# Kernel tuning notes

Hardware: AMD Instinct MI355X
Metric: run time of the kernel (lower is better)

Reference implementation:

```python
import jax, jax.numpy as jnp
import numpy as np

DIM = 768; HEADS = 12; HD = DIM // HEADS; W0 = 14; W1 = 14
NT = W0 * W1; N = NT + 1; HID = 4 * DIM; B = 64
SCALE = HD ** -0.5; EPS = 1e-6


def _rel_indices():
    # replicates DecoupledRelativePositionBias index buffers
    def rel1d(s):
        i = np.arange(s)
        return i[None, :] - i[:, None] + s - 1  # [s, s]
    h = rel1d(W0).reshape(W0, 1, W0, 1) * np.ones((1, W1, 1, W1), np.int64)
    h = (rel1d(W0).reshape(W0, 1, W0, 1) + np.zeros((1, W1, 1, W1), np.int64)).reshape(NT, NT)
    w = (rel1d(W1).reshape(1, W1, 1, W1) + np.zeros((W0, 1, W0, 1), np.int64)).reshape(NT, NT)
    def add_cls(idx, off):
        new = np.zeros((N, N), np.int64)
        new[1:, 1:] = idx
        new[0, :] = off
        new[:, 0] = off + 1
        new[0, 0] = off + 2
        return new
    return add_cls(h, 2 * W0 - 1), add_cls(w, 2 * W1 - 1)


def setup_inputs() -> dict:
    key = jax.random.key(0)
    ks = jax.random.split(key, 10)
    hi, wi = _rel_indices()
    s = 0.02
    return {
        "x": jax.random.normal(ks[0], (B, N, DIM), jnp.float32),
        "norm1_w": jnp.ones((DIM,), jnp.float32),
        "norm1_b": jnp.zeros((DIM,), jnp.float32),
        "qkv_w": jax.random.normal(ks[1], (3 * DIM, DIM), jnp.float32) * s,
        "q_bias": jax.random.normal(ks[2], (DIM,), jnp.float32) * s,
        "v_bias": jax.random.normal(ks[3], (DIM,), jnp.float32) * s,
        "proj_w": jax.random.normal(ks[4], (DIM, DIM), jnp.float32) * s,
        "proj_b": jnp.zeros((DIM,), jnp.float32),
        "rpb_high": jax.random.normal(ks[5], (2 * W0 + 2, HEADS), jnp.float32) * s,
        "rpb_width": jax.random.normal(ks[6], (2 * W1 + 2, HEADS), jnp.float32) * s,
        "norm2_w": jnp.ones((DIM,), jnp.float32),
        "norm2_b": jnp.zeros((DIM,), jnp.float32),
        "fc1_w": jax.random.normal(ks[7], (HID, DIM), jnp.float32) * s,
        "fc1_b": jnp.zeros((HID,), jnp.float32),
        "fc2_w": jax.random.normal(ks[8], (DIM, HID), jnp.float32) * s,
        "fc2_b": jnp.zeros((DIM,), jnp.float32),
        "high_idx": jnp.asarray(hi, jnp.int32),
        "width_idx": jnp.asarray(wi, jnp.int32),
    }


def _ln(x, w, b):
    mu = x.mean(-1, keepdims=True)
    var = x.var(-1, keepdims=True)  # population variance, matching unbiased=False
    return (x - mu) * jax.lax.rsqrt(var + EPS) * w + b


def reference(x, norm1_w, norm1_b, qkv_w, q_bias, v_bias, proj_w, proj_b,
              rpb_high, rpb_width, norm2_w, norm2_b, fc1_w, fc1_b, fc2_w, fc2_b,
              high_idx, width_idx):
    b, n, c = x.shape
    # --- attention branch ---
    h = _ln(x, norm1_w, norm1_b)
    qkv_bias = jnp.concatenate([q_bias, jnp.zeros_like(q_bias), v_bias])
    qkv = h @ qkv_w.T + qkv_bias                      # [B, N, 3C]
    qkv = qkv.reshape(b, n, 3, HEADS, HD).transpose(2, 0, 3, 1, 4)
    q, k, v = qkv[0] * SCALE, qkv[1], qkv[2]          # [B, H, N, hd]
    attn = jnp.einsum('bhqd,bhkd->bhqk', q.astype(jnp.float32), k.astype(jnp.float32))
    # decoupled relative position bias: two embedding gathers + add
    bias = (rpb_high[high_idx] + rpb_width[width_idx]).transpose(2, 0, 1)  # [H, N, N]
    attn = attn + bias[None].astype(attn.dtype)
    attn = jax.nn.softmax(attn, axis=-1).astype(x.dtype)
    out = jnp.einsum('bhqk,bhkd->bhqd', attn, v)
    out = out.transpose(0, 2, 1, 3).reshape(b, n, c)
    x = x + (out @ proj_w.T + proj_b)
    # --- MLP branch ---
    h2 = _ln(x, norm2_w, norm2_b)
    m = jax.nn.gelu(h2 @ fc1_w.T + fc1_b, approximate=False)
    x = x + (m @ fc2_w.T + fc2_b)
    return x
```

## Files before the change

kernel.cpp:

```cpp
#include <hip/hip_runtime.h>
#include <hip/hip_bf16.h>
#include <cstdint>

#define DIM   768
#define HEADS 12
#define HD    64
#define NTOK  197
#define BATCH 64
#define MROWS (BATCH*NTOK)
#define MPAD  12672
#define HIDN  3072
#define QSCALE 0.125f
#define LNEPS 1e-6f

typedef __bf16 bf16;
typedef __bf16 bf16x8 __attribute__((ext_vector_type(8)));
typedef __bf16 bf16x4 __attribute__((ext_vector_type(4)));
typedef float  f32x4  __attribute__((ext_vector_type(4)));

__device__ inline void gload_lds16(const void* src, void* dst) {
  __builtin_amdgcn_global_load_lds(
      (__attribute__((address_space(1))) void*)(src),
      (__attribute__((address_space(3))) void*)(dst), 16, 0, 0);
}

__global__ __launch_bounds__(256) void conv_kernel(const float* __restrict__ in,
                                                   bf16* __restrict__ out, int n4) {
  int i = blockIdx.x * 256 + threadIdx.x;
  if (i < n4) {
    float4 f = ((const float4*)in)[i];
    bf16x4 o; o.x = (bf16)f.x; o.y = (bf16)f.y; o.z = (bf16)f.z; o.w = (bf16)f.w;
    ((bf16x4*)out)[i] = o;
  }
}

__global__ __launch_bounds__(256) void bias_kernel(const float* __restrict__ rh,
                                                   const float* __restrict__ rw,
                                                   const int* __restrict__ hidx,
                                                   const int* __restrict__ widx,
                                                   float* __restrict__ bias) {
  int idx = blockIdx.x * 256 + threadIdx.x;
  const int NN = NTOK * NTOK;
  if (idx >= HEADS * NN) return;
  int h  = idx / NN;
  int ij = idx - h * NN;
  bias[idx] = rh[hidx[ij] * HEADS + h] + rw[widx[ij] * HEADS + h];
}

__global__ __launch_bounds__(256) void ln_kernel(const float* __restrict__ x,
                                                 const float* __restrict__ w,
                                                 const float* __restrict__ b,
                                                 bf16* __restrict__ out) {
  int row = blockIdx.x;
  int tid = threadIdx.x;
  const float* xr = x + (size_t)row * DIM;
  float v0 = xr[tid], v1 = xr[tid + 256], v2 = xr[tid + 512];
  float s  = v0 + v1 + v2;
  float s2 = v0 * v0 + v1 * v1 + v2 * v2;
#pragma unroll
  for (int d = 1; d < 64; d <<= 1) { s += __shfl_xor(s, d); s2 += __shfl_xor(s2, d); }
  __shared__ float red[8];
  int wv = tid >> 6, ln = tid & 63;
  if (ln == 0) { red[wv] = s; red[wv + 4] = s2; }
  __syncthreads();
  s  = red[0] + red[1] + red[2] + red[3];
  s2 = red[4] + red[5] + red[6] + red[7];
  float mean = s * (1.0f / DIM);
  float var  = s2 * (1.0f / DIM) - mean * mean;
  float rs   = rsqrtf(var + LNEPS);
  bf16* outr = out + (size_t)row * DIM;
  outr[tid]       = (bf16)((v0 - mean) * rs * w[tid]       + b[tid]);
  outr[tid + 256] = (bf16)((v1 - mean) * rs * w[tid + 256] + b[tid + 256]);
  outr[tid + 512] = (bf16)((v2 - mean) * rs * w[tid + 512] + b[tid + 512]);
}

template <int EPI>
__global__ __launch_bounds__(256, 3)
void gemm128(const bf16* __restrict__ A, const bf16* __restrict__ Bw,
             int K, int Ncols, int Ntiles,
             const float* __restrict__ p0, const float* __restrict__ p1,
             void* __restrict__ outp) {
  __shared__ __align__(16) bf16 As[128 * 64];
  __shared__ __align__(16) bf16 Bs[128 * 64];
  const int tid  = threadIdx.x;
  const int wave = tid >> 6, lane = tid & 63;
  const int wm = wave >> 1, wn = wave & 1;
  const int lr16 = lane & 15, hi16 = lane >> 4;

  const int nwg = gridDim.x;
  const int q8 = nwg >> 3, r8 = nwg & 7;
  const int xcd = blockIdx.x & 7, jj8 = blockIdx.x >> 3;
  const int chunk = (xcd < r8 ? xcd * (q8 + 1) : r8 * (q8 + 1) + (xcd - r8) * q8) + jj8;
  const int mt = chunk / Ntiles, nt = chunk - mt * Ntiles;
  const int rowBase = mt * 128;
  const int colBase = nt * 128;
  const size_t Kb = (size_t)K * 2;
  const int KT = K >> 6;

  const int s7 = lr16 & 7;
  const int colk0 = (hi16 ^ s7) * 16;
  const int colk1 = ((4 + hi16) ^ s7) * 16;
  const int rowb_a = (wm * 64 + lr16) * 128;
  const int rowb_b = (wn * 64 + lr16) * 128;

  const int srow = wave * 8 + (lane >> 3);
  const int scb  = (((lane & 7) ^ ((lane >> 3) & 7)) * 16);
  const char* aSrcP[4];
  const char* bSrcP[4];
#pragma unroll
  for (int r = 0; r < 4; ++r) {
    int ra = rowBase + r * 32 + srow;
    if (ra > MROWS - 1) ra = MROWS - 1;
    aSrcP[r] = (const char*)A + (size_t)ra * Kb + scb;
    bSrcP[r] = (const char*)Bw + (size_t)(colBase + r * 32 + srow) * Kb + scb;
  }

  f32x4 acc[4][4] = {};

  for (int t = 0; t < KT; ++t) {
    const size_t koff = (size_t)t * 128;
#pragma unroll
    for (int r = 0; r < 4; ++r)
      gload_lds16(aSrcP[r] + koff, (char*)As + (r * 32 + wave * 8) * 128);
#pragma unroll
    for (int r = 0; r < 4; ++r)
      gload_lds16(bSrcP[r] + koff, (char*)Bs + (r * 32 + wave * 8) * 128);
    __syncthreads();

    bf16x8 bfr[4][2];
#pragma unroll
    for (int n = 0; n < 4; ++n) {
      bfr[n][0] = *(const bf16x8*)((const char*)Bs + rowb_b + n * 2048 + colk0);
      bfr[n][1] = *(const bf16x8*)((const char*)Bs + rowb_b + n * 2048 + colk1);
    }
#pragma unroll
    for (int m = 0; m < 4; ++m) {
      bf16x8 a0 = *(const bf16x8*)((const char*)As + rowb_a + m * 2048 + colk0);
      bf16x8 a1 = *(const bf16x8*)((const char*)As + rowb_a + m * 2048 + colk1);
#pragma unroll
      for (int n = 0; n < 4; ++n) {
        acc[m][n] = __builtin_amdgcn_mfma_f32_16x16x32_bf16(a0, bfr[n][0], acc[m][n], 0, 0, 0);
        acc[m][n] = __builtin_amdgcn_mfma_f32_16x16x32_bf16(a1, bfr[n][1], acc[m][n], 0, 0, 0);
      }
    }
    __syncthreads();
  }

  const int rl = hi16 * 4;
  const int cl = lr16;
#pragma unroll
  for (int m = 0; m < 4; ++m) {
#pragma unroll
    for (int n = 0; n < 4; ++n) {
#pragma unroll
      for (int r = 0; r < 4; ++r) {
        int row = rowBase + wm * 64 + m * 16 + rl + r;
        int col = colBase + wn * 64 + n * 16 + cl;
        if (row >= MROWS) continue;
        float v = acc[m][n][r];
        if constexpr (EPI == 0) {
          int which = col / DIM;
          int jj = col - which * DIM;
          if (which == 0) v = (v + p0[jj]) * QSCALE;
          else if (which == 2) v = v + p1[jj];
          int bb = row / NTOK, nt2 = row - bb * NTOK;
          int h = jj >> 6, hd = jj & 63;
          ((bf16*)outp)[((size_t)(which * 768 + bb * HEADS + h) * NTOK + nt2) * 64 + hd] = (bf16)v;
        } else if constexpr (EPI == 1) {
          ((float*)outp)[(size_t)row * Ncols + col] =
              p1[(size_t)row * Ncols + col] + v + p0[col];
        } else {
          float t2 = v + p0[col];
          float g = 0.5f * t2 * (1.0f + erff(t2 * 0.70710678118654752f));
          ((bf16*)outp)[(size_t)row * Ncols + col] = (bf16)g;
        }
      }
    }
  }
}

#define VTS 232
__global__ __launch_bounds__(256, 4)
void attn_kernel(const bf16* __restrict__ qkv, const float* __restrict__ bias,
                 bf16* __restrict__ out) {
  const int bh = blockIdx.x;
  const int b = bh / HEADS, h = bh - b * HEADS;
  const bf16* qg = qkv + (size_t)bh * NTOK * HD;
  const bf16* kg = qg + (size_t)768 * NTOK * HD;
  const bf16* vg = qg + (size_t)1536 * NTOK * HD;

  __shared__ __align__(16) bf16 Vt[64 * VTS];
  __shared__ __align__(16) bf16 Ps[4][2][16 * 40];

  const int tid = threadIdx.x;
  for (int i = tid; i < NTOK * HD; i += 256) {
    int j = i >> 6, d = i & 63;
    Vt[d * VTS + j] = vg[i];
  }
  for (int i = tid; i < 64 * (VTS - NTOK); i += 256) {
    int d = i / (VTS - NTOK), j = NTOK + (i - d * (VTS - NTOK));
    Vt[d * VTS + j] = (bf16)0.0f;
  }
  __syncthreads();

  const int wave = tid >> 6, lane = tid & 63;
  const int lr = lane & 15, lg = lane >> 4;
  const int tstart = (wave == 0) ? 0 : 1 + wave * 3;
  const int tcount = (wave == 0) ? 4 : 3;
  const float* bh_bias = bias + (size_t)h * NTOK * NTOK;

  for (int ti = 0; ti < tcount; ++ti) {
    const int mi = tstart + ti;
    int qrow = mi * 16 + lr; if (qrow > NTOK - 1) qrow = NTOK - 1;
    bf16x8 aq0 = *(const bf16x8*)(qg + (size_t)qrow * 64 + lg * 8);
    bf16x8 aq1 = *(const bf16x8*)(qg + (size_t)qrow * 64 + 32 + lg * 8);

    f32x4 oacc[4] = {};
    float m[4] = {-1e30f, -1e30f, -1e30f, -1e30f};
    float l[4] = {0.f, 0.f, 0.f, 0.f};
    const int ivb = (mi * 16 + lg * 4 < NTOK) ? mi * 16 + lg * 4 : NTOK - 1;

#pragma unroll 1
    for (int kt = 0; kt < 7; ++kt) {
      const int j0 = kt * 32 + lr;
      const bf16* kp0 = kg + (size_t)(kt * 32 + lr) * 64 + lg * 8;
      const bf16* kp1 = kp0 + (size_t)16 * 64;
      f32x4 s0 = {}, s1 = {};
      s0 = __builtin_amdgcn_mfma_f32_16x16x32_bf16(aq0, *(const bf16x8*)kp0, s0, 0, 0, 0);
      s0 = __builtin_amdgcn_mfma_f32_16x16x32_bf16(aq1, *(const bf16x8*)(kp0 + 32), s0, 0, 0, 0);
      s1 = __builtin_amdgcn_mfma_f32_16x16x32_bf16(aq0, *(const bf16x8*)kp1, s1, 0, 0, 0);
      s1 = __builtin_amdgcn_mfma_f32_16x16x32_bf16(aq1, *(const bf16x8*)(kp1 + 32), s1, 0, 0, 0);

      bf16* buf = &Ps[wave][kt & 1][0];
#pragma unroll
      for (int r = 0; r < 4; ++r) {
        int iv = ivb + r; if (iv > NTOK - 1) iv = NTOK - 1;
        float sv0 = (j0 < NTOK)      ? s0[r] + bh_bias[(size_t)iv * NTOK + j0]      : -1e30f;
        float sv1 = (j0 + 16 < NTOK) ? s1[r] + bh_bias[(size_t)iv * NTOK + j0 + 16] : -1e30f;
        float cmax = fmaxf(sv0, sv1);
#pragma unroll
        for (int d = 1; d < 16; d <<= 1) cmax = fmaxf(cmax, __shfl_xor(cmax, d));
        float mnew = fmaxf(m[r], cmax);
        float scale = __expf(m[r] - mnew);
        m[r] = mnew;
        float e0 = __expf(sv0 - mnew);
        float e1 = __expf(sv1 - mnew);
        l[r] = l[r] * scale + e0 + e1;
#pragma unroll
        for (int nd = 0; nd < 4; ++nd) oacc[nd][r] *= scale;
        buf[(lg * 4 + r) * 40 + lr]      = (bf16)e0;
        buf[(lg * 4 + r) * 40 + 16 + lr] = (bf16)e1;
      }
      asm volatile("s_waitcnt lgkmcnt(0)" ::: "memory");
      __builtin_amdgcn_sched_barrier(0);
      bf16x8 pa = *(const bf16x8*)&buf[lr * 40 + lg * 8];
#pragma unroll
      for (int nd = 0; nd < 4; ++nd) {
        bf16x8 bv = *(const bf16x8*)&Vt[(nd * 16 + lr) * VTS + kt * 32 + lg * 8];
        oacc[nd] = __builtin_amdgcn_mfma_f32_16x16x32_bf16(pa, bv, oacc[nd], 0, 0, 0);
      }
    }

    float rowinv[4];
#pragma unroll
    for (int r = 0; r < 4; ++r) {
      float ls = l[r];
#pragma unroll
      for (int d = 1; d < 16; d <<= 1) ls += __shfl_xor(ls, d);
      rowinv[r] = 1.0f / ls;
    }

    bf16* Ob = &Ps[wave][0][0];
#pragma unroll
    for (int nd = 0; nd < 4; ++nd)
#pragma unroll
      for (int r = 0; r < 4; ++r)
        Ob[(lg * 4 + r) * 72 + nd * 16 + lr] = (bf16)(oacc[nd][r] * rowinv[r]);
    asm volatile("s_waitcnt lgkmcnt(0)" ::: "memory");
    __builtin_amdgcn_sched_barrier(0);
    const int rows = NTOK - mi * 16;
#pragma unroll
    for (int pass = 0; pass < 2; ++pass) {
      int orow = pass * 8 + (lane >> 3);
      if (orow < rows) {
        bf16x8 v = *(const bf16x8*)&Ob[orow * 72 + (lane & 7) * 8];
        *(bf16x8*)(out + (size_t)(b * NTOK + mi * 16 + orow) * DIM + h * 64 + (lane & 7) * 8) = v;
      }
    }
  }
}

extern "C" void kernel_launch(void* const* d_in, const int* in_sizes, int n_in,
                              void* d_out, int out_size, void* d_ws, size_t ws_size,
                              hipStream_t stream) {
  const float* x    = (const float*)d_in[0];
  const float* n1w  = (const float*)d_in[1];
  const float* n1b  = (const float*)d_in[2];
  const float* qkvw = (const float*)d_in[3];
  const float* qb   = (const float*)d_in[4];
  const float* vb   = (const float*)d_in[5];
  const float* pw   = (const float*)d_in[6];
  const float* pb   = (const float*)d_in[7];
  const float* rh   = (const float*)d_in[8];
  const float* rw   = (const float*)d_in[9];
  const float* n2w  = (const float*)d_in[10];
  const float* n2b  = (const float*)d_in[11];
  const float* f1w  = (const float*)d_in[12];
  const float* f1b  = (const float*)d_in[13];
  const float* f2w  = (const float*)d_in[14];
  const float* f2b  = (const float*)d_in[15];
  const int* hidx   = (const int*)d_in[16];
  const int* widx   = (const int*)d_in[17];

  char* ws = (char*)d_ws;
  size_t off = 0;
  auto alloc = [&](size_t bytes) {
    void* p = ws + off;
    off += (bytes + 255) & ~(size_t)255;
    return p;
  };
  bf16* wqkv  = (bf16*)alloc((size_t)2304 * 768 * 2);
  bf16* wproj = (bf16*)alloc((size_t)768 * 768 * 2);
  bf16* wfc1  = (bf16*)alloc((size_t)3072 * 768 * 2);
  bf16* wfc2  = (bf16*)alloc((size_t)768 * 3072 * 2);
  float* biasT = (float*)alloc((size_t)HEADS * NTOK * NTOK * 4);
  bf16* hbf = (bf16*)alloc((size_t)MROWS * 768 * 2);
  float* x1 = (float*)alloc((size_t)MROWS * 768 * 4);
  char* region = (char*)alloc((size_t)MPAD * HIDN * 2);
  bf16* qkv   = (bf16*)region;
  bf16* attno = (bf16*)(region + (size_t)2304 * NTOK * 64 * 2);
  bf16* mbuf  = (bf16*)region;

  conv_kernel<<<(2304 * 768 / 4 + 255) / 256, 256, 0, stream>>>(qkvw, wqkv, 2304 * 768 / 4);
  conv_kernel<<<(768 * 768 / 4 + 255) / 256, 256, 0, stream>>>(pw, wproj, 768 * 768 / 4);
  conv_kernel<<<(3072 * 768 / 4 + 255) / 256, 256, 0, stream>>>(f1w, wfc1, 3072 * 768 / 4);
  conv_kernel<<<(768 * 3072 / 4 + 255) / 256, 256, 0, stream>>>(f2w, wfc2, 768 * 3072 / 4);
  bias_kernel<<<(HEADS * NTOK * NTOK + 255) / 256, 256, 0, stream>>>(rh, rw, hidx, widx, biasT);

  const int MT = MPAD / 128;
  ln_kernel<<<MROWS, 256, 0, stream>>>(x, n1w, n1b, hbf);
  gemm128<0><<<MT * 18, 256, 0, stream>>>(hbf, wqkv, 768, 2304, 18, qb, vb, qkv);
  attn_kernel<<<768, 256, 0, stream>>>(qkv, biasT, attno);
  gemm128<1><<<MT * 6, 256, 0, stream>>>(attno, wproj, 768, 768, 6, pb, x, x1);
  ln_kernel<<<MROWS, 256, 0, stream>>>(x1, n2w, n2b, hbf);
  gemm128<2><<<MT * 24, 256, 0, stream>>>(hbf, wfc1, 768, HIDN, 24, f1b, nullptr, mbuf);
  gemm128<1><<<MT * 6, 256, 0, stream>>>(mbuf, wfc2, HIDN, 768, 6, f2b, x1, d_out);
}
```

Baseline: 433.8 us.

## Double-buffer GEMM A tiles and widen attention to eight waves with bias prefetch

The GEMM now double-buffers the A tile in LDS, issuing the next A load before computing the current tile. It uses explicit vmcnt waits and raw barriers, and raises wave priority around the MFMA block. The attention kernel moves to 512 threads (8 waves) with interleaved query-tile assignment, prefetches the next key tile's bias values into registers, and skips the online-softmax rescale when the max does not grow. These changes aim to hide global-load latency and balance work across waves, at the cost of more LDS and register pressure.

```diff
diff --git a/kernel.cpp b/kernel.cpp
--- a/kernel.cpp
+++ b/kernel.cpp
@@ -23,6 +23,12 @@
       (__attribute__((address_space(1))) void*)(src),
       (__attribute__((address_space(3))) void*)(dst), 16, 0, 0);
 }
+
+#define BAR()      asm volatile("s_barrier" ::: "memory")
+#define WAIT_LGKM0() do { asm volatile("s_waitcnt lgkmcnt(0)" ::: "memory"); \
+                          __builtin_amdgcn_sched_barrier(0); } while (0)
+#define WAIT_VM(n) do { asm volatile("s_waitcnt vmcnt(" #n ")" ::: "memory"); \
+                        __builtin_amdgcn_sched_barrier(0); } while (0)
 
 __global__ __launch_bounds__(256) void conv_kernel(const float* __restrict__ in,
                                                    bf16* __restrict__ out, int n4) {
@@ -80,7 +86,7 @@
              int K, int Ncols, int Ntiles,
              const float* __restrict__ p0, const float* __restrict__ p1,
              void* __restrict__ outp) {
-  __shared__ __align__(16) bf16 As[128 * 64];
+  __shared__ __align__(16) bf16 As[2][128 * 64];
   __shared__ __align__(16) bf16 Bs[128 * 64];
   const int tid  = threadIdx.x;
   const int wave = tid >> 6, lane = tid & 63;
@@ -115,35 +121,58 @@
     bSrcP[r] = (const char*)Bw + (size_t)(colBase + r * 32 + srow) * Kb + scb;
   }
 
-  f32x4 acc[4][4] = {};
-
-  for (int t = 0; t < KT; ++t) {
+  auto stageA = [&](int t, int buf) {
     const size_t koff = (size_t)t * 128;
 #pragma unroll
     for (int r = 0; r < 4; ++r)
-      gload_lds16(aSrcP[r] + koff, (char*)As + (r * 32 + wave * 8) * 128);
+      gload_lds16(aSrcP[r] + koff, (char*)&As[buf][0] + (r * 32 + wave * 8) * 128);
+  };
+  auto stageB = [&](int t) {
+    const size_t koff = (size_t)t * 128;
 #pragma unroll
     for (int r = 0; r < 4; ++r)
       gload_lds16(bSrcP[r] + koff, (char*)Bs + (r * 32 + wave * 8) * 128);
-    __syncthreads();
-
+  };
+
+  f32x4 acc[4][4] = {};
+
+  stageA(0, 0);
+  int cur = 0;
+  for (int t = 0; t < KT; ++t) {
+    stageB(t);
+    if (t + 1 < KT) {
+      stageA(t + 1, cur ^ 1);
+      WAIT_VM(4);
+    } else {
+      WAIT_VM(0);
+    }
+    BAR();
+
+    const char* Ab = (const char*)&As[cur][0];
     bf16x8 bfr[4][2];
 #pragma unroll
     for (int n = 0; n < 4; ++n) {
       bfr[n][0] = *(const bf16x8*)((const char*)Bs + rowb_b + n * 2048 + colk0);
       bfr[n][1] = *(const bf16x8*)((const char*)Bs + rowb_b + n * 2048 + colk1);
     }
+    bf16x8 afr[4][2];
 #pragma unroll
     for (int m = 0; m < 4; ++m) {
-      bf16x8 a0 = *(const bf16x8*)((const char*)As + rowb_a + m * 2048 + colk0);
-      bf16x8 a1 = *(const bf16x8*)((const char*)As + rowb_a + m * 2048 + colk1);
+      afr[m][0] = *(const bf16x8*)(Ab + rowb_a + m * 2048 + colk0);
+      afr[m][1] = *(const bf16x8*)(Ab + rowb_a + m * 2048 + colk1);
+    }
+    WAIT_LGKM0();
+    __builtin_amdgcn_s_setprio(1);
+#pragma unroll
+    for (int m = 0; m < 4; ++m)
 #pragma unroll
       for (int n = 0; n < 4; ++n) {
-        acc[m][n] = __builtin_amdgcn_mfma_f32_16x16x32_bf16(a0, bfr[n][0], acc[m][n], 0, 0, 0);
-        acc[m][n] = __builtin_amdgcn_mfma_f32_16x16x32_bf16(a1, bfr[n][1], acc[m][n], 0, 0, 0);
-      }
-    }
-    __syncthreads();
+        acc[m][n] = __builtin_amdgcn_mfma_f32_16x16x32_bf16(afr[m][0], bfr[n][0], acc[m][n], 0, 0, 0);
+        acc[m][n] = __builtin_amdgcn_mfma_f32_16x16x32_bf16(afr[m][1], bfr[n][1], acc[m][n], 0, 0, 0);
+      }
+    __builtin_amdgcn_s_setprio(0);
+    BAR();
+    cur ^= 1;
   }
 
   const int rl = hi16 * 4;
@@ -180,7 +209,7 @@
 }
 
 #define VTS 232
-__global__ __launch_bounds__(256, 4)
+__global__ __launch_bounds__(512, 6)
 void attn_kernel(const bf16* __restrict__ qkv, const float* __restrict__ bias,
                  bf16* __restrict__ out) {
   const int bh = blockIdx.x;
@@ -190,14 +219,14 @@
   const bf16* vg = qg + (size_t)1536 * NTOK * HD;
 
   __shared__ __align__(16) bf16 Vt[64 * VTS];
-  __shared__ __align__(16) bf16 Ps[4][2][16 * 40];
+  __shared__ __align__(16) bf16 Ps[8][2][16 * 40];
 
   const int tid = threadIdx.x;
-  for (int i = tid; i < NTOK * HD; i += 256) {
+  for (int i = tid; i < NTOK * HD; i += 512) {
     int j = i >> 6, d = i & 63;
     Vt[d * VTS + j] = vg[i];
   }
-  for (int i = tid; i < 64 * (VTS - NTOK); i += 256) {
+  for (int i = tid; i < 64 * (VTS - NTOK); i += 512) {
     int d = i / (VTS - NTOK), j = NTOK + (i - d * (VTS - NTOK));
     Vt[d * VTS + j] = (bf16)0.0f;
   }
@@ -205,12 +234,11 @@
 
   const int wave = tid >> 6, lane = tid & 63;
   const int lr = lane & 15, lg = lane >> 4;
-  const int tstart = (wave == 0) ? 0 : 1 + wave * 3;
-  const int tcount = (wave == 0) ? 4 : 3;
+  const int ntiles = (wave < 5) ? 2 : 1;
   const float* bh_bias = bias + (size_t)h * NTOK * NTOK;
 
-  for (int ti = 0; ti < tcount; ++ti) {
-    const int mi = tstart + ti;
+  for (int ti = 0; ti < ntiles; ++ti) {
+    const int mi = wave + ti * 8;
     int qrow = mi * 16 + lr; if (qrow > NTOK - 1) qrow = NTOK - 1;
     bf16x8 aq0 = *(const bf16x8*)(qg + (size_t)qrow * 64 + lg * 8);
     bf16x8 aq1 = *(const bf16x8*)(qg + (size_t)qrow * 64 + 32 + lg * 8);
@@ -218,7 +246,20 @@
     f32x4 oacc[4] = {};
     float m[4] = {-1e30f, -1e30f, -1e30f, -1e30f};
     float l[4] = {0.f, 0.f, 0.f, 0.f};
-    const int ivb = (mi * 16 + lg * 4 < NTOK) ? mi * 16 + lg * 4 : NTOK - 1;
+    int iv[4];
+#pragma unroll
+    for (int r = 0; r < 4; ++r) {
+      int i = mi * 16 + lg * 4 + r;
+      iv[r] = i < NTOK ? i : NTOK - 1;
+    }
+
+    float b0[4], b1[4];
+#pragma unroll
+    for (int r = 0; r < 4; ++r) {
+      int j0 = lr, j1 = 16 + lr;
+      b0[r] = bh_bias[(size_t)iv[r] * NTOK + j0];
+      b1[r] = bh_bias[(size_t)iv[r] * NTOK + j1];
+    }
 
 #pragma unroll 1
     for (int kt = 0; kt < 7; ++kt) {
@@ -231,23 +272,35 @@
       s1 = __builtin_amdgcn_mfma_f32_16x16x32_bf16(aq0, *(const bf16x8*)kp1, s1, 0, 0, 0);
       s1 = __builtin_amdgcn_mfma_f32_16x16x32_bf16(aq1, *(const bf16x8*)(kp1 + 32), s1, 0, 0, 0);
 
+      float nb0[4], nb1[4];
+      if (kt < 6) {
+        int jn0 = (kt + 1) * 32 + lr; if (jn0 > NTOK - 1) jn0 = NTOK - 1;
+        int jn1 = (kt + 1) * 32 + 16 + lr; if (jn1 > NTOK - 1) jn1 = NTOK - 1;
+#pragma unroll
+        for (int r = 0; r < 4; ++r) {
+          nb0[r] = bh_bias[(size_t)iv[r] * NTOK + jn0];
+          nb1[r] = bh_bias[(size_t)iv[r] * NTOK + jn1];
+        }
+      }
+
       bf16* buf = &Ps[wave][kt & 1][0];
 #pragma unroll
       for (int r = 0; r < 4; ++r) {
-        int iv = ivb + r; if (iv > NTOK - 1) iv = NTOK - 1;
-        float sv0 = (j0 < NTOK)      ? s0[r] + bh_bias[(size_t)iv * NTOK + j0]      : -1e30f;
-        float sv1 = (j0 + 16 < NTOK) ? s1[r] + bh_bias[(size_t)iv * NTOK + j0 + 16] : -1e30f;
+        float sv0 = (j0 < NTOK)      ? s0[r] + b0[r] : -1e30f;
+        float sv1 = (j0 + 16 < NTOK) ? s1[r] + b1[r] : -1e30f;
         float cmax = fmaxf(sv0, sv1);
 #pragma unroll
         for (int d = 1; d < 16; d <<= 1) cmax = fmaxf(cmax, __shfl_xor(cmax, d));
-        float mnew = fmaxf(m[r], cmax);
-        float scale = __expf(m[r] - mnew);
-        m[r] = mnew;
-        float e0 = __expf(sv0 - mnew);
-        float e1 = __expf(sv1 - mnew);
-        l[r] = l[r] * scale + e0 + e1;
-#pragma unroll
-        for (int nd = 0; nd < 4; ++nd) oacc[nd][r] *= scale;
+        if (cmax > m[r]) {
+          float scale = __expf(m[r] - cmax);
+          l[r] *= scale;
+#pragma unroll
+          for (int nd = 0; nd < 4; ++nd) oacc[nd][r] *= scale;
+          m[r] = cmax;
+        }
+        float e0 = __expf(sv0 - m[r]);
+        float e1 = __expf(sv1 - m[r]);
+        l[r] += e0 + e1;
         buf[(lg * 4 + r) * 40 + lr]      = (bf16)e0;
         buf[(lg * 4 + r) * 40 + 16 + lr] = (bf16)e1;
       }
@@ -258,6 +311,10 @@
       for (int nd = 0; nd < 4; ++nd) {
         bf16x8 bv = *(const bf16x8*)&Vt[(nd * 16 + lr) * VTS + kt * 32 + lg * 8];
         oacc[nd] = __builtin_amdgcn_mfma_f32_16x16x32_bf16(pa, bv, oacc[nd], 0, 0, 0);
+      }
+      if (kt < 6) {
+#pragma unroll
+        for (int r = 0; r < 4; ++r) { b0[r] = nb0[r]; b1[r] = nb1[r]; }
       }
     }
 
@@ -340,7 +397,7 @@
   const int MT = MPAD / 128;
   ln_kernel<<<MROWS, 256, 0, stream>>>(x, n1w, n1b, hbf);
   gemm128<0><<<MT * 18, 256, 0, stream>>>(hbf, wqkv, 768, 2304, 18, qb, vb, qkv);
-  attn_kernel<<<768, 256, 0, stream>>>(qkv, biasT, attno);
+  attn_kernel<<<768, 512, 0, stream>>>(qkv, biasT, attno);
   gemm128<1><<<MT * 6, 256, 0, stream>>>(attno, wproj, 768, 768, 6, pb, x, x1);
   ln_kernel<<<MROWS, 256, 0, stream>>>(x1, n2w, n2b, hbf);
   gemm128<2><<<MT * 24, 256, 0, stream>>>(hbf, wfc1, 768, HIDN, 24, f1b, nullptr, mbuf);
```

Measured after the change: 573.7 us. 1.32x slower.
